# Optimization experiments

Hardware: AMD Instinct MI355X
Metric: run time of the kernel (lower is better)

## Reference

```python
import jax, jax.numpy as jnp
import numpy as np

EPSILON = 0.1


def setup_inputs() -> dict:
    key = jax.random.key(0)
    ks = jax.random.split(key, 6)
    N, E, F_IN, F_OUT, NF = 50000, 800000, 256, 96, 3
    x = jax.random.normal(ks[0], (N, F_IN), dtype=jnp.float32)
    adj_vals = jax.random.uniform(ks[1], (E,), dtype=jnp.float32)
    d_scales = jax.random.uniform(ks[2], (NF, N), dtype=jnp.float32)
    # xavier-uniform-ish weights
    limit = np.sqrt(6.0 / (F_IN + F_OUT)).astype(np.float32)
    weights = jax.random.uniform(ks[3], (NF, F_IN, F_OUT), dtype=jnp.float32,
                                 minval=-limit, maxval=limit)
    bias = jnp.zeros((F_OUT,), dtype=jnp.float32)
    edge_index = jax.random.randint(ks[4], (2, E), 0, N, dtype=jnp.int32)
    return {"x": x, "adj_vals": adj_vals, "d_scales": d_scales,
            "weights": weights, "bias": bias, "edge_index": edge_index}


def reference(x, adj_vals, d_scales, weights, bias, edge_index):
    N = x.shape[0]
    row, col = edge_index[0], edge_index[1]

    # degree with self loops (add_remaining_self_loops adds 1 per node)
    deg = jax.ops.segment_sum(jnp.ones_like(adj_vals), row, num_segments=N) + 1.0
    eps_deg_inv = EPSILON / deg  # [N], diagonal of sparse_degree(..., epsilon)

    def spmm(t):  # symadj @ t via edge list
        return jax.ops.segment_sum(adj_vals[:, None] * t[col], row, num_segments=N)

    out = jnp.zeros((N, weights.shape[2]), dtype=x.dtype)
    n_filters = weights.shape[0]
    for ii in range(n_filters):
        sign = -1.0 if ii == 0 else 1.0  # Ad = symadj -/+ eps*diag(deg^-1)
        t = d_scales[ii][:, None] * (x @ weights[ii])          # D @ (x W)
        t = spmm(t) + sign * eps_deg_inv[:, None] * t          # Ad @ t
        t = d_scales[ii][:, None] * jax.nn.relu(t)             # D @ relu(t)
        out = out + t
    return out + bias
```

## Files before the change

### kernel.cpp

```cpp
#include <hip/hip_runtime.h>

#define EPSILON 0.1f
#define F_IN 256
#define F_OUT 96
#define NF 3
#define TCOLS 288
#define TSTRIDE 320
#define CAP 64
#define BN 96
#define CW 104
#define NCVT (TCOLS * F_IN / 4)

typedef __attribute__((ext_vector_type(8))) short bf8_t;
typedef __attribute__((ext_vector_type(4))) float f32x4;

__device__ inline ushort f2b(float f) {
    union { float f; unsigned u; } v; v.f = f;
    unsigned u = v.u;
    return (ushort)((u + 0x7FFFu + ((u >> 16) & 1u)) >> 16);
}
__device__ inline float blo(unsigned u) { return __uint_as_float(u << 16); }
__device__ inline float bhi(unsigned u) { return __uint_as_float(u & 0xffff0000u); }

__device__ inline bf8_t cvt8(float4 a, float4 b) {
    bf8_t r;
    r[0] = (short)f2b(a.x); r[1] = (short)f2b(a.y);
    r[2] = (short)f2b(a.z); r[3] = (short)f2b(a.w);
    r[4] = (short)f2b(b.x); r[5] = (short)f2b(b.y);
    r[6] = (short)f2b(b.z); r[7] = (short)f2b(b.w);
    return r;
}

__global__ __launch_bounds__(256) void setup_kernel(const float* __restrict__ w,
                                                    ushort* __restrict__ wt,
                                                    int* __restrict__ cnt, int N) {
    int tid = blockIdx.x * 256 + threadIdx.x;
    if (tid < NCVT) {
        int base = tid * 4;
        int gc = base >> 8;
        int k  = base & 255;
        int ii = gc / F_OUT;
        int c  = gc - ii * F_OUT;
        const float* wp = w + (size_t)ii * (F_IN * F_OUT) + (size_t)k * F_OUT + c;
        ushort4 o;
        o.x = f2b(wp[0 * F_OUT]);
        o.y = f2b(wp[1 * F_OUT]);
        o.z = f2b(wp[2 * F_OUT]);
        o.w = f2b(wp[3 * F_OUT]);
        *(ushort4*)(wt + base) = o;
    } else {
        int z = (tid - NCVT) * 4;
        if (z + 3 < N) {
            *(int4*)(cnt + z) = make_int4(0, 0, 0, 0);
        } else {
            for (int j = z; j < N && j >= 0; ++j) cnt[j] = 0;
        }
    }
}

__global__ __launch_bounds__(256) void scatter_cvt_kernel(
        const int* __restrict__ row, const int* __restrict__ col,
        const float* __restrict__ vals, int* __restrict__ cnt,
        int2* __restrict__ evs2, int E,
        const float* __restrict__ x, ushort* __restrict__ xb, int N, int nscat) {
    if ((int)blockIdx.x < nscat) {
        int i0 = (blockIdx.x * 256 + threadIdx.x) * 4;
        if (i0 + 3 < E) {
            int4   r4 = *(const int4*)(row + i0);
            int4   c4 = *(const int4*)(col + i0);
            float4 v4 = *(const float4*)(vals + i0);
            int k;
            k = atomicAdd(&cnt[r4.x], 1);
            if (k < CAP) evs2[(size_t)r4.x * CAP + k] = make_int2(c4.x, __float_as_int(v4.x));
            k = atomicAdd(&cnt[r4.y], 1);
            if (k < CAP) evs2[(size_t)r4.y * CAP + k] = make_int2(c4.y, __float_as_int(v4.y));
            k = atomicAdd(&cnt[r4.z], 1);
            if (k < CAP) evs2[(size_t)r4.z * CAP + k] = make_int2(c4.z, __float_as_int(v4.z));
            k = atomicAdd(&cnt[r4.w], 1);
            if (k < CAP) evs2[(size_t)r4.w * CAP + k] = make_int2(c4.w, __float_as_int(v4.w));
        } else {
            for (int i = i0; i < E; ++i) {
                int r = row[i];
                int k = atomicAdd(&cnt[r], 1);
                if (k < CAP) evs2[(size_t)r * CAP + k] = make_int2(col[i], __float_as_int(vals[i]));
            }
        }
    } else {
        size_t base = ((size_t)(blockIdx.x - nscat) * 256 + threadIdx.x) * 8;
        if (base < (size_t)N * F_IN) {
            float4 a = *(const float4*)(x + base);
            float4 b = *(const float4*)(x + base + 4);
            bf8_t o = cvt8(a, b);
            *(bf8_t*)(xb + base) = o;
        }
    }
}

__global__ __launch_bounds__(256) void gemm_mfma(const ushort* __restrict__ xb,
                                                 const ushort* __restrict__ wt,
                                                 const float* __restrict__ dsc,
                                                 ushort* __restrict__ t, int N) {
    __shared__ ushort Bs[BN * F_IN];

    int tid = threadIdx.x;
    int lane = tid & 63, wave = tid >> 6;
    int cl = lane & 15, quad = lane >> 4;
    int mb = blockIdx.x / 3, cb = blockIdx.x - mb * 3;
    int gc0 = cb * BN;
    int m0 = mb * 64 + wave * 16;
    int mrow = m0 + cl;
    bool aok = (mrow < N);

    #pragma unroll
    for (int i = 0; i < 12; ++i) {
        int F = tid + i * 256;
        int rem = F & 63;
        int q = rem >> 4, c = rem & 15;
        int ksj = F >> 6;
        int ks = ksj / 6, j = ksj - ks * 6;
        int gc = gc0 + j * 16 + c;
        *(uint4*)(Bs + (size_t)F * 8) =
            *(const uint4*)(wt + (size_t)gc * F_IN + ks * 32 + q * 8);
    }

    uint4 areg[8];
    const ushort* xp = xb + (size_t)mrow * F_IN + quad * 8;
    const uint4 zu = make_uint4(0, 0, 0, 0);
    #pragma unroll
    for (int ks = 0; ks < 8; ++ks)
        areg[ks] = aok ? *(const uint4*)(xp + ks * 32) : zu;

    f32x4 acc[6];
    #pragma unroll
    for (int j = 0; j < 6; ++j) acc[j] = (f32x4){0.f, 0.f, 0.f, 0.f};

    __syncthreads();

    #pragma unroll
    for (int ks = 0; ks < 8; ++ks) {
        bf8_t a = *(const bf8_t*)&areg[ks];
        const ushort* bb = Bs + ((size_t)(ks * 6) * 64 + lane) * 8;
        #pragma unroll
        for (int j = 0; j < 6; ++j) {
            bf8_t b = *(const bf8_t*)(bb + j * 64 * 8);
            acc[j] = __builtin_amdgcn_mfma_f32_16x16x32_bf16(a, b, acc[j], 0, 0, 0);
        }
    }

    __syncthreads();
    ushort* Cw = Bs + wave * (16 * CW);
    float dscv[3][4];
    #pragma unroll
    for (int ii = 0; ii < 3; ++ii)
        #pragma unroll
        for (int r = 0; r < 4; ++r) {
            int rowg = m0 + quad * 4 + r;
            dscv[ii][r] = (rowg < N) ? dsc[(size_t)ii * N + rowg] : 0.f;
        }
    #pragma unroll
    for (int j = 0; j < 6; ++j) {
        int ii = (gc0 + j * 16) / F_OUT;
        #pragma unroll
        for (int r = 0; r < 4; ++r)
            Cw[(quad * 4 + r) * CW + j * 16 + cl] = f2b(dscv[ii][r] * acc[j][r]);
    }
    #pragma unroll
    for (int it = 0; it < 3; ++it) {
        int idx = lane + it * 64;
        int r = idx / 12, ch = idx - r * 12;
        int grow = m0 + r;
        if (grow < N)
            *(uint4*)(t + (size_t)grow * TSTRIDE + gc0 + ch * 8) =
                *(const uint4*)&Cw[r * CW + ch * 8];
    }
}

__device__ inline void acc8(float* acc, uint4 a, float v) {
    acc[0] = fmaf(v, blo(a.x), acc[0]); acc[1] = fmaf(v, bhi(a.x), acc[1]);
    acc[2] = fmaf(v, blo(a.y), acc[2]); acc[3] = fmaf(v, bhi(a.y), acc[3]);
    acc[4] = fmaf(v, blo(a.z), acc[4]); acc[5] = fmaf(v, bhi(a.z), acc[5]);
    acc[6] = fmaf(v, blo(a.w), acc[6]); acc[7] = fmaf(v, bhi(a.w), acc[7]);
}

__global__ __launch_bounds__(256) void spmm_kernel(const ushort* __restrict__ t,
                                                   const int2* __restrict__ evs2,
                                                   const int* __restrict__ cnt,
                                                   const float* __restrict__ dsc,
                                                   const float* __restrict__ bias,
                                                   float* __restrict__ out, int N) {
    int lane = threadIdx.x & 63;
    int wave = threadIdx.x >> 6;
    int n = blockIdx.x * 4 + wave;
    if (n >= N) return;

    int deg = cnt[n];
    int mm = (deg < CAP) ? deg : CAP;
    int s = n * CAP, e = s + mm;
    int coff = (lane < 40) ? lane * 8 : 0;

    float acc[8];
    #pragma unroll
    for (int j = 0; j < 8; ++j) acc[j] = 0.f;

    for (int base = s; base < e; base += 64) {
        int idx = base + lane;
        int2 q = make_int2(0, 0);
        if (idx < e) q = evs2[idx];
        int m = min(64, e - base);
        int j = 0;
        for (; j + 3 < m; j += 4) {
            int c0 = __shfl(q.x, j, 64);
            int c1 = __shfl(q.x, j + 1, 64);
            int c2 = __shfl(q.x, j + 2, 64);
            int c3 = __shfl(q.x, j + 3, 64);
            float v0 = __int_as_float(__shfl(q.y, j, 64));
            float v1 = __int_as_float(__shfl(q.y, j + 1, 64));
            float v2 = __int_as_float(__shfl(q.y, j + 2, 64));
            float v3 = __int_as_float(__shfl(q.y, j + 3, 64));
            uint4 a0 = *(const uint4*)(t + (size_t)c0 * TSTRIDE + coff);
            uint4 a1 = *(const uint4*)(t + (size_t)c1 * TSTRIDE + coff);
            uint4 a2 = *(const uint4*)(t + (size_t)c2 * TSTRIDE + coff);
            uint4 a3 = *(const uint4*)(t + (size_t)c3 * TSTRIDE + coff);
            acc8(acc, a0, v0);
            acc8(acc, a1, v1);
            acc8(acc, a2, v2);
            acc8(acc, a3, v3);
        }
        for (; j < m; ++j) {
            int c = __shfl(q.x, j, 64);
            float v = __int_as_float(__shfl(q.y, j, 64));
            uint4 a = *(const uint4*)(t + (size_t)c * TSTRIDE + coff);
            acc8(acc, a, v);
        }
    }

    float sign = (lane < 12) ? -1.f : 1.f;
    float epsdi = EPSILON / (float)(deg + 1);
    int ii = lane / 12;
    float dscv = (lane < 36) ? dsc[(size_t)ii * N + n] : 0.f;
    uint4 sv = *(const uint4*)(t + (size_t)n * TSTRIDE + coff);
    float se = sign * epsdi;
    float val[8];
    {
        unsigned u;
        u = sv.x; val[0] = fmaf(se, blo(u), acc[0]); val[1] = fmaf(se, bhi(u), acc[1]);
        u = sv.y; val[2] = fmaf(se, blo(u), acc[2]); val[3] = fmaf(se, bhi(u), acc[3]);
        u = sv.z; val[4] = fmaf(se, blo(u), acc[4]); val[5] = fmaf(se, bhi(u), acc[5]);
        u = sv.w; val[6] = fmaf(se, blo(u), acc[6]); val[7] = fmaf(se, bhi(u), acc[7]);
    }
    #pragma unroll
    for (int j = 0; j < 8; ++j) val[j] = fmaxf(val[j], 0.f) * dscv;

    float res[8];
    #pragma unroll
    for (int j = 0; j < 8; ++j) {
        float r1 = __shfl(val[j], lane + 12, 64);
        float r2 = __shfl(val[j], lane + 24, 64);
        res[j] = val[j] + r1 + r2;
    }
    if (lane < 12) {
        float4 b0 = *(const float4*)(bias + lane * 8);
        float4 b1 = *(const float4*)(bias + lane * 8 + 4);
        float4 o0 = make_float4(res[0] + b0.x, res[1] + b0.y, res[2] + b0.z, res[3] + b0.w);
        float4 o1 = make_float4(res[4] + b1.x, res[5] + b1.y, res[6] + b1.z, res[7] + b1.w);
        *(float4*)(out + (size_t)n * F_OUT + lane * 8) = o0;
        *(float4*)(out + (size_t)n * F_OUT + lane * 8 + 4) = o1;
    }
}

extern "C" void kernel_launch(void* const* d_in, const int* in_sizes, int n_in,
                              void* d_out, int out_size, void* d_ws, size_t ws_size,
                              hipStream_t stream) {
    const float* x    = (const float*)d_in[0];
    const float* adj  = (const float*)d_in[1];
    const float* dsc  = (const float*)d_in[2];
    const float* w    = (const float*)d_in[3];
    const float* bias = (const float*)d_in[4];
    const int*   ei   = (const int*)d_in[5];

    int E = in_sizes[1];
    int N = in_sizes[0] / F_IN;
    const int* row = ei;
    const int* col = ei + E;
    float* out = (float*)d_out;

    char* p = (char*)d_ws;
    auto take = [&](size_t bytes) {
        char* r = p;
        p += (bytes + 255) & ~(size_t)255;
        return r;
    };
    int*    cnt  = (int*)take((size_t)N * 4);
    int2*   evs2 = (int2*)take((size_t)N * CAP * 8);
    ushort* wt   = (ushort*)take((size_t)TCOLS * F_IN * 2);
    ushort* xb   = (ushort*)take((size_t)N * F_IN * 2);
    ushort* t    = (ushort*)take(((size_t)N * TSTRIDE + 256) * 2);

    int nzero = (N + 3) / 4;
    setup_kernel<<<(NCVT + nzero + 255) / 256, 256, 0, stream>>>(w, wt, cnt, N);

    int nscat = (E / 4 + 255) / 256;
    int ncvtx = ((N * F_IN / 8) + 255) / 256;
    scatter_cvt_kernel<<<nscat + ncvtx, 256, 0, stream>>>(row, col, adj, cnt, evs2, E,
                                                          x, xb, N, nscat);
    gemm_mfma<<<3 * ((N + 63) / 64), 256, 0, stream>>>(xb, wt, dsc, t, N);
    spmm_kernel<<<(N + 3) / 4, 256, 0, stream>>>(t, evs2, cnt, dsc, bias, out, N);
}
```

Measured before the change: 264.2 us.

## Replace per-edge global atomic scatter with two-pass block-binned edge bucketing

Edge insertion into per-row buckets is rewritten as a two-level counting sort. Each block first histograms and locally sorts 4096 edges by 64-row bin in shared memory, then writes them contiguously to global bins. A new bucket kernel expands each bin into per-row slots in shared memory. This replaces random global atomics and scattered 8-byte writes with coalesced writes, at the cost of an extra kernel launch, an intermediate buffer, and assumptions such as column indices fitting in 16 bits and a fixed bin count and capacity.

```diff
diff --git a/kernel.cpp b/kernel.cpp
--- a/kernel.cpp
+++ b/kernel.cpp
@@ -11,6 +11,11 @@
 #define CW 104
 #define NCVT (TCOLS * F_IN / 4)
 
+#define RPB 64
+#define NBINS 782
+#define BCAP 1536
+#define EPB 4096
+
 typedef __attribute__((ext_vector_type(8))) short bf8_t;
 typedef __attribute__((ext_vector_type(4))) float f32x4;
 
@@ -33,7 +38,7 @@
 
 __global__ __launch_bounds__(256) void setup_kernel(const float* __restrict__ w,
                                                     ushort* __restrict__ wt,
-                                                    int* __restrict__ cnt, int N) {
+                                                    int* __restrict__ gcur) {
     int tid = blockIdx.x * 256 + threadIdx.x;
     if (tid < NCVT) {
         int base = tid * 4;
@@ -50,49 +55,166 @@
         *(ushort4*)(wt + base) = o;
     } else {
         int z = (tid - NCVT) * 4;
-        if (z + 3 < N) {
-            *(int4*)(cnt + z) = make_int4(0, 0, 0, 0);
+        if (z + 3 < NBINS) {
+            *(int4*)(gcur + z) = make_int4(0, 0, 0, 0);
         } else {
-            for (int j = z; j < N && j >= 0; ++j) cnt[j] = 0;
-        }
-    }
-}
-
-__global__ __launch_bounds__(256) void scatter_cvt_kernel(
+            for (int j = z; j < NBINS && j >= 0; ++j) gcur[j] = 0;
+        }
+    }
+}
+
+__global__ __launch_bounds__(256) void bin_cvt_kernel(
         const int* __restrict__ row, const int* __restrict__ col,
-        const float* __restrict__ vals, int* __restrict__ cnt,
-        int2* __restrict__ evs2, int E,
-        const float* __restrict__ x, ushort* __restrict__ xb, int N, int nscat) {
-    if ((int)blockIdx.x < nscat) {
-        int i0 = (blockIdx.x * 256 + threadIdx.x) * 4;
-        if (i0 + 3 < E) {
-            int4   r4 = *(const int4*)(row + i0);
-            int4   c4 = *(const int4*)(col + i0);
-            float4 v4 = *(const float4*)(vals + i0);
-            int k;
-            k = atomicAdd(&cnt[r4.x], 1);
-            if (k < CAP) evs2[(size_t)r4.x * CAP + k] = make_int2(c4.x, __float_as_int(v4.x));
-            k = atomicAdd(&cnt[r4.y], 1);
-            if (k < CAP) evs2[(size_t)r4.y * CAP + k] = make_int2(c4.y, __float_as_int(v4.y));
-            k = atomicAdd(&cnt[r4.z], 1);
-            if (k < CAP) evs2[(size_t)r4.z * CAP + k] = make_int2(c4.z, __float_as_int(v4.z));
-            k = atomicAdd(&cnt[r4.w], 1);
-            if (k < CAP) evs2[(size_t)r4.w * CAP + k] = make_int2(c4.w, __float_as_int(v4.w));
-        } else {
-            for (int i = i0; i < E; ++i) {
-                int r = row[i];
-                int k = atomicAdd(&cnt[r], 1);
-                if (k < CAP) evs2[(size_t)r * CAP + k] = make_int2(col[i], __float_as_int(vals[i]));
+        const float* __restrict__ vals, int E,
+        int* __restrict__ gcur, int2* __restrict__ gout,
+        const float* __restrict__ x, ushort* __restrict__ xb, int N, int nbin) {
+    __shared__ int2 ord[EPB];
+    __shared__ int hist[NBINS];
+    __shared__ int gbase[NBINS];
+    __shared__ int basex[NBINS];
+    __shared__ int ts[512];
+
+    if ((int)blockIdx.x < nbin) {
+        int tid = threadIdx.x;
+        for (int i = tid; i < NBINS; i += 256) hist[i] = 0;
+        __syncthreads();
+
+        int e0 = (int)blockIdx.x * EPB;
+        int4 r4[4], c4[4]; float4 v4[4];
+        int rank[16], binv[16], valv[16];
+        unsigned recx[16];
+        #pragma unroll
+        for (int g = 0; g < 4; ++g) {
+            int e = e0 + tid * 4 + g * 1024;
+            if (e + 3 < E) {
+                r4[g] = *(const int4*)(row + e);
+                c4[g] = *(const int4*)(col + e);
+                v4[g] = *(const float4*)(vals + e);
+            } else {
+                int4 rr, cc; float4 vv;
+                int* rp = (int*)&rr; int* cp = (int*)&cc; float* vp = (float*)&vv;
+                #pragma unroll
+                for (int j = 0; j < 4; ++j) {
+                    int ee = e + j;
+                    rp[j] = (ee < E) ? row[ee] : -1;
+                    cp[j] = (ee < E) ? col[ee] : 0;
+                    vp[j] = (ee < E) ? vals[ee] : 0.f;
+                }
+                r4[g] = rr; c4[g] = cc; v4[g] = vv;
             }
         }
+        #pragma unroll
+        for (int g = 0; g < 4; ++g) {
+            const int* rp = (const int*)&r4[g];
+            const int* cp = (const int*)&c4[g];
+            const float* vp = (const float*)&v4[g];
+            #pragma unroll
+            for (int j = 0; j < 4; ++j) {
+                int s = g * 4 + j;
+                int r = rp[j];
+                if (r >= 0) {
+                    int b = r >> 6;
+                    binv[s] = b;
+                    recx[s] = (unsigned)(cp[j] & 0xffff) |
+                              ((unsigned)(r & 63) << 16) | ((unsigned)b << 22);
+                    valv[s] = __float_as_int(vp[j]);
+                    rank[s] = atomicAdd(&hist[b], 1);
+                } else {
+                    binv[s] = -1; rank[s] = 0; recx[s] = 0; valv[s] = 0;
+                }
+            }
+        }
+        __syncthreads();
+
+        int b0 = tid * 4;
+        int h0 = (b0     < NBINS) ? hist[b0]     : 0;
+        int h1 = (b0 + 1 < NBINS) ? hist[b0 + 1] : 0;
+        int h2 = (b0 + 2 < NBINS) ? hist[b0 + 2] : 0;
+        int h3 = (b0 + 3 < NBINS) ? hist[b0 + 3] : 0;
+        int tot = h0 + h1 + h2 + h3;
+        ts[tid] = tot;
+        __syncthreads();
+        int src = 0;
+        #pragma unroll
+        for (int off = 1; off < 256; off <<= 1) {
+            int v = ts[src * 256 + tid];
+            if (tid >= off) v += ts[src * 256 + tid - off];
+            ts[(src ^ 1) * 256 + tid] = v;
+            __syncthreads();
+            src ^= 1;
+        }
+        int excl = ts[src * 256 + tid] - tot;
+        if (b0     < NBINS) basex[b0]     = excl;
+        if (b0 + 1 < NBINS) basex[b0 + 1] = excl + h0;
+        if (b0 + 2 < NBINS) basex[b0 + 2] = excl + h0 + h1;
+        if (b0 + 3 < NBINS) basex[b0 + 3] = excl + h0 + h1 + h2;
+        #pragma unroll
+        for (int q = 0; q < 4; ++q) {
+            int i = b0 + q;
+            if (i < NBINS) {
+                int h = hist[i];
+                gbase[i] = h ? atomicAdd(&gcur[i], h) : 0;
+            }
+        }
+        __syncthreads();
+
+        #pragma unroll
+        for (int s = 0; s < 16; ++s)
+            if (binv[s] >= 0)
+                ord[basex[binv[s]] + rank[s]] = make_int2((int)recx[s], valv[s]);
+        __syncthreads();
+
+        int total = ts[src * 256 + 255];
+        for (int i = tid; i < total; i += 256) {
+            int2 rec = ord[i];
+            int b = ((unsigned)rec.x) >> 22;
+            int pos = gbase[b] + (i - basex[b]);
+            if (pos < BCAP)
+                gout[(size_t)b * BCAP + pos] = rec;
+        }
     } else {
-        size_t base = ((size_t)(blockIdx.x - nscat) * 256 + threadIdx.x) * 8;
+        size_t base = ((size_t)((int)blockIdx.x - nbin) * 256 + threadIdx.x) * 8;
         if (base < (size_t)N * F_IN) {
             float4 a = *(const float4*)(x + base);
             float4 b = *(const float4*)(x + base + 4);
             bf8_t o = cvt8(a, b);
             *(bf8_t*)(xb + base) = o;
         }
+    }
+}
+
+__global__ __launch_bounds__(256) void bucket_kernel(
+        const int2* __restrict__ gout, const int* __restrict__ gcur,
+        int* __restrict__ cnt, int2* __restrict__ evs2, int N) {
+    __shared__ int2 buck[RPB * CAP];
+    __shared__ int lcnt[RPB];
+
+    int tid = threadIdx.x;
+    int b = blockIdx.x;
+    if (tid < RPB) lcnt[tid] = 0;
+    __syncthreads();
+
+    int nrec = gcur[b];
+    if (nrec > BCAP) nrec = BCAP;
+    for (int i = tid; i < nrec; i += 256) {
+        int2 rec = gout[(size_t)b * BCAP + i];
+        int rl = (rec.x >> 16) & 63;
+        int c  = rec.x & 0xffff;
+        int k = atomicAdd(&lcnt[rl], 1);
+        if (k < CAP) buck[rl * CAP + k] = make_int2(c, rec.y);
+    }
+    __syncthreads();
+
+    int row0 = b * RPB;
+    if (tid < RPB && row0 + tid < N) cnt[row0 + tid] = lcnt[tid];
+
+    int lane = tid & 63, wave = tid >> 6;
+    for (int r = wave; r < RPB; r += 4) {
+        int rowg = row0 + r;
+        if (rowg >= N) break;
+        int m = min(lcnt[r], CAP);
+        if (lane < m)
+            evs2[(size_t)rowg * CAP + lane] = buck[r * CAP + lane];
     }
 }
 
@@ -295,14 +417,17 @@
     ushort* wt   = (ushort*)take((size_t)TCOLS * F_IN * 2);
     ushort* xb   = (ushort*)take((size_t)N * F_IN * 2);
     ushort* t    = (ushort*)take(((size_t)N * TSTRIDE + 256) * 2);
-
-    int nzero = (N + 3) / 4;
-    setup_kernel<<<(NCVT + nzero + 255) / 256, 256, 0, stream>>>(w, wt, cnt, N);
-
-    int nscat = (E / 4 + 255) / 256;
+    int*    gcur = (int*)take((size_t)NBINS * 4);
+    int2*   gout = (int2*)take((size_t)NBINS * BCAP * 8);
+
+    int nzero = (NBINS + 3) / 4;
+    setup_kernel<<<(NCVT + nzero + 255) / 256, 256, 0, stream>>>(w, wt, gcur);
+
+    int nbin  = (E + EPB - 1) / EPB;
     int ncvtx = ((N * F_IN / 8) + 255) / 256;
-    scatter_cvt_kernel<<<nscat + ncvtx, 256, 0, stream>>>(row, col, adj, cnt, evs2, E,
-                                                          x, xb, N, nscat);
+    bin_cvt_kernel<<<nbin + ncvtx, 256, 0, stream>>>(row, col, adj, E, gcur, gout,
+                                                     x, xb, N, nbin);
+    bucket_kernel<<<NBINS, 256, 0, stream>>>(gout, gcur, cnt, evs2, N);
     gemm_mfma<<<3 * ((N + 63) / 64), 256, 0, stream>>>(xb, wt, dsc, t, N);
     spmm_kernel<<<(N + 3) / 4, 256, 0, stream>>>(t, evs2, cnt, dsc, bias, out, N);
 }
```

New measurement: 231.5 us. -12.4%, faster.
